# Performance work log

Hardware: AMD Instinct MI355X
Metric: run time of the kernel (lower is better)

## Reference

```python
import jax, jax.numpy as jnp
import numpy as np

B, T, N_EMBD = 1, 2048, 2048
N_HEAD = 16
KV_LOW = 512      # kv_low_rank == head_size (compressed value dim)
Q_LOW = 1024
ROPE_HS = 64
QK_HS = KV_LOW + ROPE_HS  # 576
HEAD_SIZE = KV_LOW        # v_equiv = c_kv.view(B,1,T,head_size)


def _rope_tables(seq_len, dim, base=10000.0):
    # litgpt-style: theta over half dim, duplicated to full dim
    inv = 1.0 / (base ** (np.arange(0, dim, 2, dtype=np.float32) / dim))
    t = np.arange(seq_len, dtype=np.float32)
    freqs = np.outer(t, inv)                      # [T, dim/2]
    emb = np.concatenate([freqs, freqs], axis=-1)  # [T, dim]
    return jnp.asarray(np.cos(emb)), jnp.asarray(np.sin(emb))


def _apply_rope(x, cos, sin):
    # x: [..., T, d]; cos/sin broadcastable [T, d]. rotate-half RoPE.
    d = x.shape[-1]
    x1, x2 = x[..., : d // 2], x[..., d // 2:]
    rotated = jnp.concatenate([-x2, x1], axis=-1)
    return x * cos + rotated * sin


def setup_inputs() -> dict:
    key = jax.random.key(0)
    ks = jax.random.split(key, 4)
    x = jax.random.normal(ks[0], (B, T, N_EMBD), dtype=jnp.float32)
    cos, sin = _rope_tables(T, ROPE_HS)
    s = 0.02
    W_qkv = jax.random.normal(ks[1], (N_EMBD, KV_LOW + ROPE_HS + Q_LOW), dtype=jnp.float32) * s
    W_qdec = jax.random.normal(ks[2], (Q_LOW, N_HEAD * QK_HS), dtype=jnp.float32) * s
    W_out = jax.random.normal(ks[3], (N_HEAD * HEAD_SIZE, N_EMBD), dtype=jnp.float32) * s
    return {"x": x, "cos": cos, "sin": sin, "W_qkv": W_qkv, "W_qdec": W_qdec, "W_out": W_out}


def reference(x, cos, sin, W_qkv, W_qdec, W_out):
    Bq, Tq, _ = x.shape
    # latent encoding and split
    latents = x @ W_qkv                                       # [B,T,kv+rope+q]
    c_kv = latents[..., :KV_LOW]                              # [B,T,512] (keys-nope and values)
    k_r = latents[..., KV_LOW:KV_LOW + ROPE_HS]               # [B,T,64]
    c_q = latents[..., KV_LOW + ROPE_HS:]                     # [B,T,1024]
    # per-head query decode
    q = (c_q @ W_qdec).reshape(Bq, Tq, N_HEAD, QK_HS)         # [B,T,H,576]
    q_nope, q_r = q[..., :KV_LOW], q[..., KV_LOW:]
    # partial RoPE
    k_r = _apply_rope(k_r, cos, sin)                          # [B,T,64]
    q_r = _apply_rope(q_r, cos[None, :, None, :], sin[None, :, None, :])  # [B,T,H,64]
    q = jnp.concatenate([q_nope, q_r], axis=-1)               # [B,T,H,576]
    q = jnp.swapaxes(q, 1, 2)                                 # [B,H,T,576]
    k = jnp.concatenate([c_kv, k_r], axis=-1)                 # [B,T,576] shared across heads
    v = c_kv                                                  # [B,T,512] shared across heads
    scale = 1.0 / jnp.sqrt(jnp.float32(HEAD_SIZE))
    scores = jnp.einsum('bhtd,bsd->bhts', q, k) * scale       # [B,H,T,T]
    causal = jnp.tril(jnp.ones((Tq, Tq), dtype=bool))
    scores = jnp.where(causal, scores, jnp.finfo(scores.dtype).min)
    attn = jax.nn.softmax(scores, axis=-1)
    y = jnp.einsum('bhts,bsd->bhtd', attn, v)                 # [B,H,T,512]
    y = jnp.swapaxes(y, 1, 2).reshape(Bq, Tq, N_HEAD * HEAD_SIZE)
    return y @ W_out                                          # [B,T,n_embd]
```

## Files before the change

### kernel.cpp

```cpp
#include <hip/hip_runtime.h>

typedef __bf16 bf16x8_t __attribute__((ext_vector_type(8)));
typedef float f32x4_t __attribute__((ext_vector_type(4)));

#define LAT_LD 1664
#define QK_DIM 576
#define V_DIM 512
#define NHEAD 16
#define TSEQ 2048
#define QLD 9216
#define YLD 8192
#define KLD 576
#define SCALE 0.044194173824159216f

__device__ __forceinline__ unsigned short f2bf(float f) {
  union { float f; unsigned int u; } v; v.f = f;
  unsigned int r = v.u + 0x7FFFu + ((v.u >> 16) & 1u);
  return (unsigned short)(r >> 16);
}

__device__ __forceinline__ void load_lds16(const unsigned short* g, unsigned short* l) {
  __builtin_amdgcn_global_load_lds((const __attribute__((address_space(1))) void*)g,
                                   (__attribute__((address_space(3))) void*)l, 16, 0, 0);
}

__device__ __forceinline__ void conv_t_body(const float* __restrict__ src, int R, int Csrc,
                                            unsigned short* __restrict__ dst,
                                            int bx, int by, int tid,
                                            unsigned short (*T)[72]) {
  const int r0 = bx * 64, c0 = by * 64;
  const bool live = (c0 < Csrc);
#pragma unroll
  for (int it = 0; it < 4; ++it) {
    int idx = it * 256 + tid;
    int c4 = (idx >> 6) * 4;
    int r = idx & 63;
    float4 v = {0.f, 0.f, 0.f, 0.f};
    if (live) v = *(const float4*)&src[(size_t)(r0 + r) * Csrc + c0 + c4];
    T[c4 + 0][r] = f2bf(v.x);
    T[c4 + 1][r] = f2bf(v.y);
    T[c4 + 2][r] = f2bf(v.z);
    T[c4 + 3][r] = f2bf(v.w);
  }
  __syncthreads();
#pragma unroll
  for (int it = 0; it < 2; ++it) {
    int idx = it * 256 + tid;
    int cc = idx >> 3, r8 = (idx & 7) * 8;
    uint4 v = *(const uint4*)&T[cc][r8];
    *(uint4*)&dst[(size_t)(c0 + cc) * R + r0 + r8] = v;
  }
}

__global__ __launch_bounds__(256) void prep_all(
    const float* __restrict__ x, unsigned short* __restrict__ xb,
    const float* __restrict__ wqkv, unsigned short* __restrict__ wqkvT,
    const float* __restrict__ wqdec, unsigned short* __restrict__ wqdecT,
    const float* __restrict__ wout, unsigned short* __restrict__ woutT,
    float* __restrict__ lsum) {
  __shared__ unsigned short T[64][72];
  const int blk = blockIdx.x, tid = threadIdx.x;
  if (blk < 4096) {
    int i = (blk * 256 + tid) * 4;
    float4 v = *(const float4*)&x[i];
    ushort4 o;
    o.x = f2bf(v.x); o.y = f2bf(v.y); o.z = f2bf(v.z); o.w = f2bf(v.w);
    *(ushort4*)&xb[i] = o;
  } else if (blk < 4928) {
    int l = blk - 4096;
    conv_t_body(wqkv, 2048, 1600, wqkvT, l & 31, l >> 5, tid, T);
  } else if (blk < 7232) {
    int l = blk - 4928;
    conv_t_body(wqdec, 1024, 9216, wqdecT, l & 15, l >> 4, tid, T);
  } else if (blk < 11328) {
    int l = blk - 7232;
    conv_t_body(wout, 8192, 2048, woutT, l & 127, l >> 7, tid, T);
  } else {
    int i = ((blk - 11328) * 256 + tid) * 4;
    *(float4*)&lsum[i] = (float4){0.f, 0.f, 0.f, 0.f};
  }
}

__global__ __launch_bounds__(256) void vtrans_kcopy(const unsigned short* __restrict__ lat,
                                                    unsigned short* __restrict__ vtg,
                                                    unsigned short* __restrict__ kbuf) {
  __shared__ unsigned short T[64][72];
  const int tid = threadIdx.x;
  const int r0 = blockIdx.x * 64, c0 = blockIdx.y * 64;
#pragma unroll
  for (int it = 0; it < 2; ++it) {
    int idx = it * 256 + tid;
    int c8 = (idx >> 6) * 8;
    int r = idx & 63;
    uint4 v = *(const uint4*)&lat[(size_t)(r0 + r) * LAT_LD + c0 + c8];
    *(uint4*)&kbuf[(size_t)(r0 + r) * KLD + c0 + c8] = v;
    unsigned short* pv = (unsigned short*)&v;
#pragma unroll
    for (int j = 0; j < 8; ++j) T[c8 + j][r] = pv[j];
  }
  __syncthreads();
#pragma unroll
  for (int it = 0; it < 2; ++it) {
    int idx = it * 256 + tid;
    int cc = idx >> 3, r8 = (idx & 7) * 8;
    uint4 v = *(const uint4*)&T[cc][r8];
    *(uint4*)&vtg[(size_t)(c0 + cc) * TSEQ + r0 + r8] = v;
  }
}

__global__ __launch_bounds__(256) void rope_k(const unsigned short* __restrict__ lat,
                                              unsigned short* __restrict__ kbuf,
                                              const float* __restrict__ cosb,
                                              const float* __restrict__ sinb) {
  int idx = blockIdx.x * 256 + threadIdx.x;
  if (idx >= TSEQ * 32) return;
  int t = idx >> 5, d = idx & 31;
  const unsigned short* p = &lat[(size_t)t * LAT_LD + 512];
  union { unsigned int u; float f; } a, b;
  a.u = ((unsigned int)p[d]) << 16; b.u = ((unsigned int)p[d + 32]) << 16;
  float c0 = cosb[t * 64 + d], s0 = sinb[t * 64 + d];
  float c1 = cosb[t * 64 + d + 32], s1 = sinb[t * 64 + d + 32];
  kbuf[(size_t)t * KLD + 512 + d] = f2bf(a.f * c0 - b.f * s0);
  kbuf[(size_t)t * KLD + 544 + d] = f2bf(b.f * c1 + a.f * s1);
}

#define GEMM_PROLOGUE()                                                     \
  __shared__ __align__(16) unsigned short As[4096];                         \
  __shared__ __align__(16) unsigned short Bs[4096];                         \
  const int tid = threadIdx.x;                                              \
  const int wave = tid >> 6, lane = tid & 63;                               \
  const int quad = lane >> 4, l16 = lane & 15;                              \
  const int wm = wave >> 1, wn = wave & 1;                                  \
  f32x4_t acc[4][4];                                                        \
  f32x4_t zero = {0.f, 0.f, 0.f, 0.f};                                      \
  _Pragma("unroll") for (int mi = 0; mi < 4; ++mi)                          \
    _Pragma("unroll") for (int ni = 0; ni < 4; ++ni) acc[mi][ni] = zero;

#define GEMM_KLOOP(Aptr, Alda, Bptr, Bldb, M0, N0, KLEN)                    \
  for (int k0 = 0; k0 < (KLEN); k0 += 32) {                                 \
    _Pragma("unroll") for (int p2 = 0; p2 < 2; ++p2) {                      \
      int ci = p2 * 256 + tid;                                              \
      int rr2 = ci >> 2, cc2 = (ci & 3) * 8;                                \
      load_lds16(&(Aptr)[(size_t)((M0) + rr2) * (Alda) + k0 + cc2], &As[ci * 8]); \
      load_lds16(&(Bptr)[(size_t)((N0) + rr2) * (Bldb) + k0 + cc2], &Bs[ci * 8]); \
    }                                                                       \
    __syncthreads();                                                        \
    bf16x8_t af[4], bfr[4];                                                 \
    _Pragma("unroll") for (int mi = 0; mi < 4; ++mi)                        \
      af[mi] = *(const bf16x8_t*)&As[(wm * 64 + mi * 16 + l16) * 32 + quad * 8]; \
    _Pragma("unroll") for (int ni = 0; ni < 4; ++ni)                        \
      bfr[ni] = *(const bf16x8_t*)&Bs[(wn * 64 + ni * 16 + l16) * 32 + quad * 8]; \
    _Pragma("unroll") for (int mi = 0; mi < 4; ++mi)                        \
      _Pragma("unroll") for (int ni = 0; ni < 4; ++ni)                      \
        acc[mi][ni] = __builtin_amdgcn_mfma_f32_16x16x32_bf16(af[mi], bfr[ni], acc[mi][ni], 0, 0, 0); \
    __syncthreads();                                                        \
  }

__global__ __launch_bounds__(256, 2) void gemm_splitk(
    const unsigned short* __restrict__ A, int lda,
    const unsigned short* __restrict__ Bt, int ldb,
    float* __restrict__ P, int ldc, int Ks) {
  const int m0 = blockIdx.y * 128, n0 = blockIdx.x * 128;
  const size_t koff = (size_t)blockIdx.z * Ks;
  const unsigned short* Ap = A + koff;
  const unsigned short* Bp = Bt + koff;
  float* C = P + (size_t)blockIdx.z * ((size_t)gridDim.y * 128) * ldc;
  GEMM_PROLOGUE();
  GEMM_KLOOP(Ap, lda, Bp, ldb, m0, n0, Ks);
#pragma unroll
  for (int mi = 0; mi < 4; ++mi)
#pragma unroll
    for (int ni = 0; ni < 4; ++ni)
#pragma unroll
      for (int r = 0; r < 4; ++r) {
        int row = m0 + wm * 64 + mi * 16 + quad * 4 + r;
        int col = n0 + wn * 64 + ni * 16 + l16;
        C[(size_t)row * ldc + col] = acc[mi][ni][r];
      }
}

__global__ __launch_bounds__(256, 2) void gemm_qdec(
    const unsigned short* __restrict__ A,
    const unsigned short* __restrict__ Bt,
    unsigned short* __restrict__ qbuf,
    const float* __restrict__ cosb, const float* __restrict__ sinb) {
  const int m0 = blockIdx.y * 128, n0 = blockIdx.x * 128;
  GEMM_PROLOGUE();
  GEMM_KLOOP(A, LAT_LD, Bt, 1024, m0, n0, 1024);

  const int cb = n0 + wn * 64;
  const bool ropeh = (cb % QK_DIM) == 512;
#pragma unroll
  for (int mi = 0; mi < 4; ++mi)
#pragma unroll
    for (int r = 0; r < 4; ++r) {
      int t = m0 + wm * 64 + mi * 16 + quad * 4 + r;
      if (ropeh) {
#pragma unroll
        for (int ni = 0; ni < 2; ++ni) {
          int d = ni * 16 + l16;
          float c0f = cosb[t * 64 + d], s0f = sinb[t * 64 + d];
          float c1f = cosb[t * 64 + d + 32], s1f = sinb[t * 64 + d + 32];
          float v1 = acc[mi][ni][r], v2 = acc[mi][ni + 2][r];
          qbuf[(size_t)t * QLD + cb + d] = f2bf(v1 * c0f - v2 * s0f);
          qbuf[(size_t)t * QLD + cb + 32 + d] = f2bf(v2 * c1f + v1 * s1f);
        }
      } else {
#pragma unroll
        for (int ni = 0; ni < 4; ++ni)
          qbuf[(size_t)t * QLD + cb + ni * 16 + l16] = f2bf(acc[mi][ni][r]);
      }
    }
}

__global__ __launch_bounds__(256) void reduce2_bf(const float* __restrict__ p,
                                                  unsigned short* __restrict__ dst, int n) {
  int i = (blockIdx.x * 256 + threadIdx.x) * 4;
  if (i < n) {
    float4 a = *(const float4*)&p[i];
    float4 b = *(const float4*)&p[(size_t)n + i];
    ushort4 o;
    o.x = f2bf(a.x + b.x); o.y = f2bf(a.y + b.y);
    o.z = f2bf(a.z + b.z); o.w = f2bf(a.w + b.w);
    *(ushort4*)&dst[i] = o;
  }
}

__global__ __launch_bounds__(256) void reduce4_f32(const float* __restrict__ p,
                                                   float* __restrict__ dst, int n) {
  int i = (blockIdx.x * 256 + threadIdx.x) * 4;
  if (i < n) {
    float4 a = *(const float4*)&p[i];
    float4 b = *(const float4*)&p[(size_t)n + i];
    float4 c = *(const float4*)&p[2 * (size_t)n + i];
    float4 d = *(const float4*)&p[3 * (size_t)n + i];
    float4 o;
    o.x = (a.x + b.x) + (c.x + d.x);
    o.y = (a.y + b.y) + (c.y + d.y);
    o.z = (a.z + b.z) + (c.z + d.z);
    o.w = (a.w + b.w) + (c.w + d.w);
    *(float4*)&dst[i] = o;
  }
}

__global__ __launch_bounds__(256, 2) void qke_kernel(
    const unsigned short* __restrict__ qbuf,
    const unsigned short* __restrict__ kbuf,
    unsigned short* __restrict__ Ebuf,
    float* __restrict__ lsum, int tq0, int tq1) {
  int tx = blockIdx.x, ig = tq1 - 1, cnt = tq1;
  while (tx >= cnt) { tx -= cnt; --ig; --cnt; }
  const int j = tx;
  const int h = blockIdx.y;
  const int Kmax = (ig + 1) << 7;
  const int r0g = ig << 7;
  const int panelSz = (tq1 * (tq1 + 1) - tq0 * (tq0 + 1)) >> 1;
  const int pre = (ig * (ig + 1) - tq0 * (tq0 + 1)) >> 1;

  const unsigned short* A = qbuf + (size_t)r0g * QLD + h * QK_DIM;
  const unsigned short* Bt = kbuf + (size_t)(j << 7) * KLD;
  unsigned short* Eh = Ebuf + ((size_t)h * panelSz + pre) * 16384;

  GEMM_PROLOGUE();
  GEMM_KLOOP(A, QLD, Bt, KLD, 0, 0, QK_DIM);

#pragma unroll
  for (int mi = 0; mi < 4; ++mi) {
    float rs[4] = {0.f, 0.f, 0.f, 0.f};
#pragma unroll
    for (int ni = 0; ni < 4; ++ni)
#pragma unroll
      for (int r = 0; r < 4; ++r) {
        int qr = r0g + wm * 64 + mi * 16 + quad * 4 + r;
        int key = (j << 7) + wn * 64 + ni * 16 + l16;
        float e = (key <= qr) ? __expf(acc[mi][ni][r] * SCALE) : 0.f;
        rs[r] += e;
        Eh[(size_t)(qr - r0g) * Kmax + key] = f2bf(e);
      }
#pragma unroll
    for (int r = 0; r < 4; ++r) {
      float s = rs[r];
#pragma unroll
      for (int off = 1; off < 16; off <<= 1) s += __shfl_xor(s, off, 64);
      if (l16 == 0) {
        int qr = r0g + wm * 64 + mi * 16 + quad * 4 + r;
        atomicAdd(&lsum[h * TSEQ + qr], s);
      }
    }
  }
}

__global__ __launch_bounds__(256, 2) void pv_kernel(
    const unsigned short* __restrict__ Ebuf,
    const unsigned short* __restrict__ vtg,
    const float* __restrict__ lsum,
    unsigned short* __restrict__ ybuf, int tq0, int tq1) {
  const int i_l = (tq1 - tq0 - 1) - blockIdx.y;
  const int ig = tq0 + i_l;
  const int h = blockIdx.z;
  const int n0 = blockIdx.x * 128;
  const int Kmax = (ig + 1) << 7;
  const int panelSz = (tq1 * (tq1 + 1) - tq0 * (tq0 + 1)) >> 1;
  const int pre = (ig * (ig + 1) - tq0 * (tq0 + 1)) >> 1;

  const unsigned short* A = Ebuf + ((size_t)h * panelSz + pre) * 16384;

  GEMM_PROLOGUE();
  GEMM_KLOOP(A, Kmax, vtg, TSEQ, 0, n0, Kmax);

#pragma unroll
  for (int mi = 0; mi < 4; ++mi)
#pragma unroll
    for (int r = 0; r < 4; ++r) {
      int row_g = (ig << 7) + wm * 64 + mi * 16 + quad * 4 + r;
      float inv = 1.f / lsum[h * TSEQ + row_g];
#pragma unroll
      for (int ni = 0; ni < 4; ++ni) {
        int col = h * V_DIM + n0 + wn * 64 + ni * 16 + l16;
        ybuf[(size_t)row_g * YLD + col] = f2bf(acc[mi][ni][r] * inv);
      }
    }
}

extern "C" void kernel_launch(void* const* d_in, const int* in_sizes, int n_in,
                              void* d_out, int out_size, void* d_ws, size_t ws_size,
                              hipStream_t stream) {
  (void)in_sizes; (void)n_in; (void)out_size; (void)ws_size;
  const float* x     = (const float*)d_in[0];
  const float* cosb  = (const float*)d_in[1];
  const float* sinb  = (const float*)d_in[2];
  const float* wqkv  = (const float*)d_in[3];
  const float* wqdec = (const float*)d_in[4];
  const float* wout  = (const float*)d_in[5];
  float* out = (float*)d_out;

  unsigned short* ws     = (unsigned short*)d_ws;
  unsigned short* xb     = ws;
  unsigned short* wqkvT  = xb     + (size_t)2048 * 2048;
  unsigned short* wqdecT = wqkvT  + (size_t)1664 * 2048;
  unsigned short* lat    = wqdecT + (size_t)9216 * 1024;
  unsigned short* qbuf   = lat    + (size_t)2048 * 1664;
  unsigned short* woutT  = qbuf   + (size_t)2048 * 9216;
  unsigned short* ybuf   = woutT  + (size_t)2048 * 8192;
  unsigned short* vtg    = ybuf   + (size_t)2048 * 8192;
  unsigned short* kbuf   = vtg    + (size_t)512 * 2048;
  float*          lsumf  = (float*)(kbuf + (size_t)2048 * 576);
  unsigned short* Ebuf   = ws;
  float*          P1     = (float*)qbuf;
  float*          Pf     = (float*)ws;

  prep_all<<<11360, 256, 0, stream>>>(x, xb, wqkv, wqkvT, wqdec, wqdecT, wout, woutT, lsumf);

  gemm_splitk<<<dim3(13, 16, 2), 256, 0, stream>>>(xb, 2048, wqkvT, 2048, P1, 1664, 1024);
  reduce2_bf<<<3328, 256, 0, stream>>>(P1, lat, 2048 * 1664);
  rope_k<<<256, 256, 0, stream>>>(lat, kbuf, cosb, sinb);
  vtrans_kcopy<<<dim3(32, 8), 256, 0, stream>>>(lat, vtg, kbuf);

  gemm_qdec<<<dim3(72, 16), 256, 0, stream>>>(lat + 576, wqdecT, qbuf, cosb, sinb);

  qke_kernel<<<dim3(66, 16), 256, 0, stream>>>(qbuf, kbuf, Ebuf, lsumf, 0, 11);
  pv_kernel<<<dim3(4, 11, 16), 256, 0, stream>>>(Ebuf, vtg, lsumf, ybuf, 0, 11);
  qke_kernel<<<dim3(70, 16), 256, 0, stream>>>(qbuf, kbuf, Ebuf, lsumf, 11, 16);
  pv_kernel<<<dim3(4, 5, 16), 256, 0, stream>>>(Ebuf, vtg, lsumf, ybuf, 11, 16);

  gemm_splitk<<<dim3(16, 16, 4), 256, 0, stream>>>(ybuf, YLD, woutT, 8192, Pf, 2048, 2048);
  reduce4_f32<<<4096, 256, 0, stream>>>(Pf, out, 2048 * 2048);
}
```

Before: 544.8 us.

## Fuse latent post-processing, deepen GEMM K-step, split attention by head groups

Merges the split-K reduction, RoPE on k, K copy and V transpose into one postlat kernel, so the latent buffer is not written and re-read between three separate launches. The shared GEMM macro now stages 64 K-elements per barrier instead of 32, which halves the number of synchronisations per tile at the cost of double the LDS per block (32 KB). The attention phase is split into two passes of 8 heads over all query tiles instead of two passes over query-tile ranges, giving each launch an even amount of work. The transpose-load index order is also changed for better coalescing.

```diff
diff --git a/kernel.cpp b/kernel.cpp
--- a/kernel.cpp
+++ b/kernel.cpp
@@ -33,8 +33,7 @@
 #pragma unroll
   for (int it = 0; it < 4; ++it) {
     int idx = it * 256 + tid;
-    int c4 = (idx >> 6) * 4;
-    int r = idx & 63;
+    int r = idx >> 4, c4 = (idx & 15) * 4;
     float4 v = {0.f, 0.f, 0.f, 0.f};
     if (live) v = *(const float4*)&src[(size_t)(r0 + r) * Csrc + c0 + c4];
     T[c4 + 0][r] = f2bf(v.x);
@@ -81,52 +80,67 @@
   }
 }
 
-__global__ __launch_bounds__(256) void vtrans_kcopy(const unsigned short* __restrict__ lat,
-                                                    unsigned short* __restrict__ vtg,
-                                                    unsigned short* __restrict__ kbuf) {
+__global__ __launch_bounds__(256) void postlat(
+    const float* __restrict__ P1,
+    unsigned short* __restrict__ lat,
+    unsigned short* __restrict__ kbuf,
+    unsigned short* __restrict__ vtg,
+    const float* __restrict__ cosb, const float* __restrict__ sinb) {
   __shared__ unsigned short T[64][72];
   const int tid = threadIdx.x;
-  const int r0 = blockIdx.x * 64, c0 = blockIdx.y * 64;
-#pragma unroll
-  for (int it = 0; it < 2; ++it) {
+  const int bx = blockIdx.x, by = blockIdx.y;
+  const int r0 = bx * 64, c0 = by * 64;
+  const size_t n = (size_t)2048 * 1664;
+
+#pragma unroll
+  for (int it = 0; it < 4; ++it) {
     int idx = it * 256 + tid;
-    int c8 = (idx >> 6) * 8;
-    int r = idx & 63;
-    uint4 v = *(const uint4*)&lat[(size_t)(r0 + r) * LAT_LD + c0 + c8];
-    *(uint4*)&kbuf[(size_t)(r0 + r) * KLD + c0 + c8] = v;
-    unsigned short* pv = (unsigned short*)&v;
-#pragma unroll
-    for (int j = 0; j < 8; ++j) T[c8 + j][r] = pv[j];
-  }
+    int r = idx >> 4, c4 = (idx & 15) * 4;
+    size_t off = (size_t)(r0 + r) * 1664 + c0 + c4;
+    float4 a = *(const float4*)&P1[off];
+    float4 b = *(const float4*)&P1[n + off];
+    ushort4 o;
+    o.x = f2bf(a.x + b.x); o.y = f2bf(a.y + b.y);
+    o.z = f2bf(a.z + b.z); o.w = f2bf(a.w + b.w);
+    if (by < 8) {
+      *(ushort4*)&kbuf[(size_t)(r0 + r) * KLD + c0 + c4] = o;
+      T[c4 + 0][r] = o.x; T[c4 + 1][r] = o.y; T[c4 + 2][r] = o.z; T[c4 + 3][r] = o.w;
+    } else if (by == 8) {
+      T[r][c4 + 0] = o.x; T[r][c4 + 1] = o.y; T[r][c4 + 2] = o.z; T[r][c4 + 3] = o.w;
+    } else {
+      *(ushort4*)&lat[(size_t)(r0 + r) * LAT_LD + c0 + c4] = o;
+    }
+  }
+  if (by > 8) return;
   __syncthreads();
-#pragma unroll
-  for (int it = 0; it < 2; ++it) {
-    int idx = it * 256 + tid;
-    int cc = idx >> 3, r8 = (idx & 7) * 8;
-    uint4 v = *(const uint4*)&T[cc][r8];
-    *(uint4*)&vtg[(size_t)(c0 + cc) * TSEQ + r0 + r8] = v;
-  }
-}
-
-__global__ __launch_bounds__(256) void rope_k(const unsigned short* __restrict__ lat,
-                                              unsigned short* __restrict__ kbuf,
-                                              const float* __restrict__ cosb,
-                                              const float* __restrict__ sinb) {
-  int idx = blockIdx.x * 256 + threadIdx.x;
-  if (idx >= TSEQ * 32) return;
-  int t = idx >> 5, d = idx & 31;
-  const unsigned short* p = &lat[(size_t)t * LAT_LD + 512];
-  union { unsigned int u; float f; } a, b;
-  a.u = ((unsigned int)p[d]) << 16; b.u = ((unsigned int)p[d + 32]) << 16;
-  float c0 = cosb[t * 64 + d], s0 = sinb[t * 64 + d];
-  float c1 = cosb[t * 64 + d + 32], s1 = sinb[t * 64 + d + 32];
-  kbuf[(size_t)t * KLD + 512 + d] = f2bf(a.f * c0 - b.f * s0);
-  kbuf[(size_t)t * KLD + 544 + d] = f2bf(b.f * c1 + a.f * s1);
+  if (by < 8) {
+#pragma unroll
+    for (int it = 0; it < 2; ++it) {
+      int idx = it * 256 + tid;
+      int cc = idx >> 3, r8 = (idx & 7) * 8;
+      uint4 v = *(const uint4*)&T[cc][r8];
+      *(uint4*)&vtg[(size_t)(c0 + cc) * TSEQ + r0 + r8] = v;
+    }
+  } else {
+#pragma unroll
+    for (int it = 0; it < 8; ++it) {
+      int idx = it * 256 + tid;
+      int r = idx >> 5, d = idx & 31;
+      int t = r0 + r;
+      union { unsigned int u; float f; } a, b;
+      a.u = ((unsigned int)T[r][d]) << 16;
+      b.u = ((unsigned int)T[r][d + 32]) << 16;
+      float c0f = cosb[t * 64 + d], s0f = sinb[t * 64 + d];
+      float c1f = cosb[t * 64 + d + 32], s1f = sinb[t * 64 + d + 32];
+      kbuf[(size_t)t * KLD + 512 + d] = f2bf(a.f * c0f - b.f * s0f);
+      kbuf[(size_t)t * KLD + 544 + d] = f2bf(b.f * c1f + a.f * s1f);
+    }
+  }
 }
 
 #define GEMM_PROLOGUE()                                                     \
-  __shared__ __align__(16) unsigned short As[4096];                         \
-  __shared__ __align__(16) unsigned short Bs[4096];                         \
+  __shared__ __align__(16) unsigned short As[8192];                         \
+  __shared__ __align__(16) unsigned short Bs[8192];                         \
   const int tid = threadIdx.x;                                              \
   const int wave = tid >> 6, lane = tid & 63;                               \
   const int quad = lane >> 4, l16 = lane & 15;                              \
@@ -137,22 +151,28 @@
     _Pragma("unroll") for (int ni = 0; ni < 4; ++ni) acc[mi][ni] = zero;
 
 #define GEMM_KLOOP(Aptr, Alda, Bptr, Bldb, M0, N0, KLEN)                    \
-  for (int k0 = 0; k0 < (KLEN); k0 += 32) {                                 \
+  for (int k0 = 0; k0 < (KLEN); k0 += 64) {                                 \
     _Pragma("unroll") for (int p2 = 0; p2 < 2; ++p2) {                      \
       int ci = p2 * 256 + tid;                                              \
       int rr2 = ci >> 2, cc2 = (ci & 3) * 8;                                \
-      load_lds16(&(Aptr)[(size_t)((M0) + rr2) * (Alda) + k0 + cc2], &As[ci * 8]); \
-      load_lds16(&(Bptr)[(size_t)((N0) + rr2) * (Bldb) + k0 + cc2], &Bs[ci * 8]); \
+      const unsigned short* ga = &(Aptr)[(size_t)((M0) + rr2) * (Alda) + k0 + cc2]; \
+      const unsigned short* gb = &(Bptr)[(size_t)((N0) + rr2) * (Bldb) + k0 + cc2]; \
+      load_lds16(ga,      &As[ci * 8]);                                     \
+      load_lds16(ga + 32, &As[4096 + ci * 8]);                              \
+      load_lds16(gb,      &Bs[ci * 8]);                                     \
+      load_lds16(gb + 32, &Bs[4096 + ci * 8]);                              \
     }                                                                       \
     __syncthreads();                                                        \
-    bf16x8_t af[4], bfr[4];                                                 \
-    _Pragma("unroll") for (int mi = 0; mi < 4; ++mi)                        \
-      af[mi] = *(const bf16x8_t*)&As[(wm * 64 + mi * 16 + l16) * 32 + quad * 8]; \
-    _Pragma("unroll") for (int ni = 0; ni < 4; ++ni)                        \
-      bfr[ni] = *(const bf16x8_t*)&Bs[(wn * 64 + ni * 16 + l16) * 32 + quad * 8]; \
-    _Pragma("unroll") for (int mi = 0; mi < 4; ++mi)                        \
+    _Pragma("unroll") for (int hf = 0; hf < 2; ++hf) {                      \
+      bf16x8_t af[4], bfr[4];                                               \
+      _Pragma("unroll") for (int mi = 0; mi < 4; ++mi)                      \
+        af[mi] = *(const bf16x8_t*)&As[hf * 4096 + (wm * 64 + mi * 16 + l16) * 32 + quad * 8]; \
       _Pragma("unroll") for (int ni = 0; ni < 4; ++ni)                      \
-        acc[mi][ni] = __builtin_amdgcn_mfma_f32_16x16x32_bf16(af[mi], bfr[ni], acc[mi][ni], 0, 0, 0); \
+        bfr[ni] = *(const bf16x8_t*)&Bs[hf * 4096 + (wn * 64 + ni * 16 + l16) * 32 + quad * 8]; \
+      _Pragma("unroll") for (int mi = 0; mi < 4; ++mi)                      \
+        _Pragma("unroll") for (int ni = 0; ni < 4; ++ni)                    \
+          acc[mi][ni] = __builtin_amdgcn_mfma_f32_16x16x32_bf16(af[mi], bfr[ni], acc[mi][ni], 0, 0, 0); \
+    }                                                                       \
     __syncthreads();                                                        \
   }
 
@@ -211,19 +231,6 @@
           qbuf[(size_t)t * QLD + cb + ni * 16 + l16] = f2bf(acc[mi][ni][r]);
       }
     }
-}
-
-__global__ __launch_bounds__(256) void reduce2_bf(const float* __restrict__ p,
-                                                  unsigned short* __restrict__ dst, int n) {
-  int i = (blockIdx.x * 256 + threadIdx.x) * 4;
-  if (i < n) {
-    float4 a = *(const float4*)&p[i];
-    float4 b = *(const float4*)&p[(size_t)n + i];
-    ushort4 o;
-    o.x = f2bf(a.x + b.x); o.y = f2bf(a.y + b.y);
-    o.z = f2bf(a.z + b.z); o.w = f2bf(a.w + b.w);
-    *(ushort4*)&dst[i] = o;
-  }
 }
 
 __global__ __launch_bounds__(256) void reduce4_f32(const float* __restrict__ p,
@@ -247,19 +254,18 @@
     const unsigned short* __restrict__ qbuf,
     const unsigned short* __restrict__ kbuf,
     unsigned short* __restrict__ Ebuf,
-    float* __restrict__ lsum, int tq0, int tq1) {
-  int tx = blockIdx.x, ig = tq1 - 1, cnt = tq1;
+    float* __restrict__ lsum, int hbase) {
+  int tx = blockIdx.x, ig = 15, cnt = 16;
   while (tx >= cnt) { tx -= cnt; --ig; --cnt; }
   const int j = tx;
-  const int h = blockIdx.y;
+  const int hl = blockIdx.y, h = hbase + hl;
   const int Kmax = (ig + 1) << 7;
   const int r0g = ig << 7;
-  const int panelSz = (tq1 * (tq1 + 1) - tq0 * (tq0 + 1)) >> 1;
-  const int pre = (ig * (ig + 1) - tq0 * (tq0 + 1)) >> 1;
+  const int pre = (ig * (ig + 1)) >> 1;
 
   const unsigned short* A = qbuf + (size_t)r0g * QLD + h * QK_DIM;
   const unsigned short* Bt = kbuf + (size_t)(j << 7) * KLD;
-  unsigned short* Eh = Ebuf + ((size_t)h * panelSz + pre) * 16384;
+  unsigned short* Eh = Ebuf + ((size_t)hl * 136 + pre) * 16384;
 
   GEMM_PROLOGUE();
   GEMM_KLOOP(A, QLD, Bt, KLD, 0, 0, QK_DIM);
@@ -294,16 +300,14 @@
     const unsigned short* __restrict__ Ebuf,
     const unsigned short* __restrict__ vtg,
     const float* __restrict__ lsum,
-    unsigned short* __restrict__ ybuf, int tq0, int tq1) {
-  const int i_l = (tq1 - tq0 - 1) - blockIdx.y;
-  const int ig = tq0 + i_l;
-  const int h = blockIdx.z;
+    unsigned short* __restrict__ ybuf, int hbase) {
+  const int ig = 15 - blockIdx.y;
+  const int hl = blockIdx.z, h = hbase + hl;
   const int n0 = blockIdx.x * 128;
   const int Kmax = (ig + 1) << 7;
-  const int panelSz = (tq1 * (tq1 + 1) - tq0 * (tq0 + 1)) >> 1;
-  const int pre = (ig * (ig + 1) - tq0 * (tq0 + 1)) >> 1;
-
-  const unsigned short* A = Ebuf + ((size_t)h * panelSz + pre) * 16384;
+  const int pre = (ig * (ig + 1)) >> 1;
+
+  const unsigned short* A = Ebuf + ((size_t)hl * 136 + pre) * 16384;
 
   GEMM_PROLOGUE();
   GEMM_KLOOP(A, Kmax, vtg, TSEQ, 0, n0, Kmax);
@@ -352,16 +356,14 @@
   prep_all<<<11360, 256, 0, stream>>>(x, xb, wqkv, wqkvT, wqdec, wqdecT, wout, woutT, lsumf);
 
   gemm_splitk<<<dim3(13, 16, 2), 256, 0, stream>>>(xb, 2048, wqkvT, 2048, P1, 1664, 1024);
-  reduce2_bf<<<3328, 256, 0, stream>>>(P1, lat, 2048 * 1664);
-  rope_k<<<256, 256, 0, stream>>>(lat, kbuf, cosb, sinb);
-  vtrans_kcopy<<<dim3(32, 8), 256, 0, stream>>>(lat, vtg, kbuf);
+  postlat<<<dim3(32, 26), 256, 0, stream>>>(P1, lat, kbuf, vtg, cosb, sinb);
 
   gemm_qdec<<<dim3(72, 16), 256, 0, stream>>>(lat + 576, wqdecT, qbuf, cosb, sinb);
 
-  qke_kernel<<<dim3(66, 16), 256, 0, stream>>>(qbuf, kbuf, Ebuf, lsumf, 0, 11);
-  pv_kernel<<<dim3(4, 11, 16), 256, 0, stream>>>(Ebuf, vtg, lsumf, ybuf, 0, 11);
-  qke_kernel<<<dim3(70, 16), 256, 0, stream>>>(qbuf, kbuf, Ebuf, lsumf, 11, 16);
-  pv_kernel<<<dim3(4, 5, 16), 256, 0, stream>>>(Ebuf, vtg, lsumf, ybuf, 11, 16);
+  qke_kernel<<<dim3(136, 8), 256, 0, stream>>>(qbuf, kbuf, Ebuf, lsumf, 0);
+  pv_kernel<<<dim3(4, 16, 8), 256, 0, stream>>>(Ebuf, vtg, lsumf, ybuf, 0);
+  qke_kernel<<<dim3(136, 8), 256, 0, stream>>>(qbuf, kbuf, Ebuf, lsumf, 8);
+  pv_kernel<<<dim3(4, 16, 8), 256, 0, stream>>>(Ebuf, vtg, lsumf, ybuf, 8);
 
   gemm_splitk<<<dim3(16, 16, 4), 256, 0, stream>>>(ybuf, YLD, woutT, 8192, Pf, 2048, 2048);
   reduce4_f32<<<4096, 256, 0, stream>>>(Pf, out, 2048 * 2048);
```

Measured after the change: 505.5 us. 1.08x faster.
